# Optimization experiments

Hardware: AMD Instinct MI355X
Metric: run time of the kernel (lower is better)

Reference implementation:

```python
import jax, jax.numpy as jnp
import numpy as np

HEADS = 12
HEAD_SIZE = 64
NEG_BIG = 1e12


def _rope_sin_cos(seq_len, head_size, dtype):
    # embeddings[n, 2i] = sin(n * 10000^(-2i/d)), [n, 2i+1] = cos(...)
    pos = jnp.arange(seq_len, dtype=dtype)                      # [s]
    idx = jnp.arange(head_size // 2, dtype=dtype)               # [d/2]
    inv_freq = jnp.power(jnp.asarray(10000.0, dtype), -2.0 * idx / head_size)
    ang = jnp.einsum('n,d->nd', pos, inv_freq)                  # [s, d/2]
    # cos_pos / sin_pos: repeat_interleave each frequency twice -> [1, s, 1, d]
    cos = jnp.repeat(jnp.cos(ang), 2, axis=-1)[None, :, None, :]
    sin = jnp.repeat(jnp.sin(ang), 2, axis=-1)[None, :, None, :]
    return sin, cos


def _rotate_half_interleaved(x):
    # stack([-x[..., 1::2], x[..., ::2]], -1).reshape_as(x)
    x2 = jnp.stack([-x[..., 1::2], x[..., ::2]], axis=-1)
    return x2.reshape(x.shape)


def setup_inputs() -> dict:
    key = jax.random.key(0)
    k1, k2 = jax.random.split(key)
    bs, s, h = 16, 512, 768
    hidden = jax.random.normal(k1, (bs, s, h), dtype=jnp.float32)
    attention_mask = jnp.ones((bs, s), dtype=jnp.int32)
    W = jax.random.normal(k2, (h, HEADS * 2 * HEAD_SIZE), dtype=jnp.float32) * (h ** -0.5)
    b = jnp.zeros((HEADS * 2 * HEAD_SIZE,), dtype=jnp.float32)
    return {"hidden": hidden, "attention_mask": attention_mask, "W": W, "b": b}


def reference(hidden, attention_mask, W, b):
    bs, s, _ = hidden.shape
    x = hidden @ W + b                                           # [b, s, heads*2*hd]
    x = x.reshape(bs, s, HEADS, 2, HEAD_SIZE)
    qw, kw = x[..., 0, :], x[..., 1, :]                          # [b, s, h, d]

    sin, cos = _rope_sin_cos(s, HEAD_SIZE, hidden.dtype)
    qw = qw * cos + _rotate_half_interleaved(qw) * sin
    kw = kw * cos + _rotate_half_interleaved(kw) * sin

    logits = jnp.einsum('bmhd,bnhd->bhmn', qw, kw)               # [b, h, s, s]

    am = attention_mask.astype(logits.dtype)
    pad_mask = 1.0 - am[:, None, None, :] * am[:, None, :, None]
    logits = logits - pad_mask * NEG_BIG

    tril = jnp.tril(jnp.ones((s, s), dtype=logits.dtype), k=-1)  # strictly lower
    logits = logits - tril[None, None, :, :] * NEG_BIG

    return logits / (HEAD_SIZE ** 0.5)
```

## Files before the change

kernel.cpp:

```cpp
#include <hip/hip_runtime.h>
#include <math.h>

#define HEADS 12
#define HSZ   64
#define SEQ   512
#define HID   768
#define NOUT  1536
#define NEGQ  1.25e11f

typedef _Float16 f16x8 __attribute__((ext_vector_type(8)));
typedef _Float16 f16x4 __attribute__((ext_vector_type(4)));
typedef float    f32x4 __attribute__((ext_vector_type(4)));
typedef int      i32x4 __attribute__((ext_vector_type(4)));
typedef int      i32x8 __attribute__((ext_vector_type(8)));

__device__ __forceinline__ void async_ld16(const void* g, void* l) {
  __builtin_amdgcn_global_load_lds(
      (__attribute__((address_space(1))) void*)g,
      (__attribute__((address_space(3))) void*)l, 16, 0, 0);
}

__global__ __launch_bounds__(256) void prep_k(
    const float* __restrict__ hidden, const float* __restrict__ W,
    unsigned char* __restrict__ Xb8, unsigned char* __restrict__ Wt8,
    float2* __restrict__ tab)
{
  __shared__ float t_lds[32][33];
  const int b = blockIdx.x;
  const int t = threadIdx.x;
  if (b < 1152) {
    const int tk = b % 24, tn = b / 24;
    const int k0 = tk * 32, n0 = tn * 32;
    const int tx = t & 31, ty = t >> 5;
#pragma unroll
    for (int r = 0; r < 4; ++r)
      t_lds[ty + r * 8][tx] = W[(size_t)(k0 + ty + r * 8) * NOUT + n0 + tx];
    __syncthreads();
    const int nl = t >> 3, kg = t & 7;
    int w = __builtin_amdgcn_cvt_pk_fp8_f32(t_lds[kg * 4 + 0][nl],
                                            t_lds[kg * 4 + 1][nl], 0, false);
    w = __builtin_amdgcn_cvt_pk_fp8_f32(t_lds[kg * 4 + 2][nl],
                                        t_lds[kg * 4 + 3][nl], w, true);
    *(int*)&Wt8[(size_t)(n0 + nl) * HID + k0 + kg * 4] = w;
  } else if (b < 1152 + 1536) {
    const int idx = (b - 1152) * 256 + t;
    const float4* src = (const float4*)hidden + (size_t)idx * 4;
    float4 v0 = src[0], v1 = src[1], v2 = src[2], v3 = src[3];
    int4 o;
    o.x = __builtin_amdgcn_cvt_pk_fp8_f32(v0.x, v0.y, 0, false);
    o.x = __builtin_amdgcn_cvt_pk_fp8_f32(v0.z, v0.w, o.x, true);
    o.y = __builtin_amdgcn_cvt_pk_fp8_f32(v1.x, v1.y, 0, false);
    o.y = __builtin_amdgcn_cvt_pk_fp8_f32(v1.z, v1.w, o.y, true);
    o.z = __builtin_amdgcn_cvt_pk_fp8_f32(v2.x, v2.y, 0, false);
    o.z = __builtin_amdgcn_cvt_pk_fp8_f32(v2.z, v2.w, o.z, true);
    o.w = __builtin_amdgcn_cvt_pk_fp8_f32(v3.x, v3.y, 0, false);
    o.w = __builtin_amdgcn_cvt_pk_fp8_f32(v3.z, v3.w, o.w, true);
    ((int4*)Xb8)[idx] = o;
  } else {
    const int e = (b - 2688) * 256 + t;
    const int si = e >> 5, fi = e & 31;
    float inv = powf(10000.f, -(float)fi / 32.f);
    float ang = (float)si * inv;
    float sv, cv;
    sincosf(ang, &sv, &cv);
    tab[e] = make_float2(cv, sv);
  }
}

__global__ __launch_bounds__(256) void gemm1_k(
    const unsigned char* __restrict__ Xb8, const unsigned char* __restrict__ Wt8,
    const float* __restrict__ bias, const float2* __restrict__ tab,
    _Float16* __restrict__ qb, _Float16* __restrict__ kb)
{
  __shared__ __align__(16) int As4[4096];
  __shared__ __align__(16) int Bs4[4096];
  const int tid = threadIdx.x;
  const int lane = tid & 63;
  const int m0 = blockIdx.x * 128;
  const int n0 = blockIdx.y * 128;
  const int wm = ((tid >> 6) & 1) * 64;
  const int wn = (tid >> 7) * 64;
  const int lrow = lane & 15;
  const int q = lane >> 4;

  f32x4 acc[4][4] = {};

  for (int kt = 0; kt < 6; ++kt) {
    const int kbase = kt * 128;
#pragma unroll
    for (int c = 0; c < 4; ++c) {
      const int s = tid + c * 256;
      const int row = s >> 3, cc = s & 7;
      const int so = (((cc >> 1) ^ (row & 3)) << 5) + ((cc & 1) << 4);
      async_ld16(Xb8 + (size_t)(m0 + row) * HID + kbase + so, (char*)As4 + s * 16);
      async_ld16(Wt8 + (size_t)(n0 + row) * HID + kbase + so, (char*)Bs4 + s * 16);
    }
    __syncthreads();
    i32x8 af[4], bf[4];
#pragma unroll
    for (int i = 0; i < 4; ++i) {
      const int ra = wm + i * 16 + lrow;
      const int oa = ra * 32 + ((q ^ (ra & 3)) << 3);
      i32x4 lo = *(const i32x4*)&As4[oa];
      i32x4 hi = *(const i32x4*)&As4[oa + 4];
      af[i] = (i32x8){lo.x, lo.y, lo.z, lo.w, hi.x, hi.y, hi.z, hi.w};
      const int rb = wn + i * 16 + lrow;
      const int ob = rb * 32 + ((q ^ (rb & 3)) << 3);
      lo = *(const i32x4*)&Bs4[ob];
      hi = *(const i32x4*)&Bs4[ob + 4];
      bf[i] = (i32x8){lo.x, lo.y, lo.z, lo.w, hi.x, hi.y, hi.z, hi.w};
    }
#pragma unroll
    for (int i = 0; i < 4; ++i)
#pragma unroll
      for (int j = 0; j < 4; ++j)
        acc[i][j] = __builtin_amdgcn_mfma_scale_f32_16x16x128_f8f6f4(
            bf[j], af[i], acc[i][j], 0, 0,
            0, 0x7F7F7F7F, 0, 0x7F7F7F7F);
    __syncthreads();
  }

  const int qlane = lane >> 4;
  const int mlane = m0 + wm + (lane & 15);
#pragma unroll
  for (int j = 0; j < 4; ++j) {
    const int nb = n0 + wn + j * 16 + qlane * 4;
    const float4 b4 = *(const float4*)&bias[nb];
    const int d0 = nb & 63;
    const int h = nb >> 7;
    _Float16* dst = ((nb >> 6) & 1) ? kb : qb;
    const int fi0 = d0 >> 1;
#pragma unroll
    for (int i = 0; i < 4; ++i) {
      const int m = mlane + i * 16;
      const int si = m & (SEQ - 1);
      const int bb = m >> 9;
      const float4 cs = *(const float4*)&tab[si * 32 + fi0];
      const float v0 = acc[i][j][0] + b4.x;
      const float v1 = acc[i][j][1] + b4.y;
      const float v2 = acc[i][j][2] + b4.z;
      const float v3 = acc[i][j][3] + b4.w;
      f16x4 o;
      o.x = (_Float16)fmaf(v0, cs.x, -v1 * cs.y);
      o.y = (_Float16)fmaf(v1, cs.x, v0 * cs.y);
      o.z = (_Float16)fmaf(v2, cs.z, -v3 * cs.w);
      o.w = (_Float16)fmaf(v3, cs.z, v2 * cs.w);
      *(f16x4*)&dst[((size_t)(bb * HEADS + h) * SEQ + si) * HSZ + d0] = o;
    }
  }
}

__global__ __launch_bounds__(256) void gemm2_k(
    const _Float16* __restrict__ qb, const _Float16* __restrict__ kb,
    const int* __restrict__ am, float* __restrict__ out)
{
  const int tid = threadIdx.x;
  const int bh = blockIdx.y;
  const int bb = bh / HEADS;
  const int mt = blockIdx.x >> 2, nt = blockIdx.x & 3;
  const int m0 = mt * 128, n0 = nt * 128;
  const int* amb = am + bb * SEQ;
  float* obase = out + (size_t)bh * SEQ * SEQ;

  if (nt < mt) {
#pragma unroll
    for (int p = 0; p < 16; ++p) {
      const int f = p * 256 + tid;
      const int row = f >> 5, c4 = (f & 31) * 4;
      const int m = m0 + row;
      const float amm = (float)amb[m];
      const int nb = n0 + c4;
      const int4 a4 = *(const int4*)&amb[nb];
      f32x4 v;
      v[0] = -(2.f - amm * (float)a4.x) * NEGQ;
      v[1] = -(2.f - amm * (float)a4.y) * NEGQ;
      v[2] = -(2.f - amm * (float)a4.z) * NEGQ;
      v[3] = -(2.f - amm * (float)a4.w) * NEGQ;
      __builtin_nontemporal_store(v, (f32x4*)&obase[(size_t)m * SEQ + nb]);
    }
    return;
  }

  const _Float16* qg = qb + (size_t)bh * SEQ * HSZ;
  const _Float16* kg = kb + (size_t)bh * SEQ * HSZ;
  const int lane = tid & 63;
  const int wm = ((tid >> 6) & 1) * 64;
  const int wn = (tid >> 7) * 64;
  const int lrow = lane & 15;
  const int lk = (lane >> 4) * 8;

  f16x8 af[4][2], bf[4][2];
#pragma unroll
  for (int i = 0; i < 4; ++i)
#pragma unroll
    for (int h = 0; h < 2; ++h) {
      af[i][h] = *(const f16x8*)(qg + (size_t)(m0 + wm + i * 16 + lrow) * HSZ + h * 32 + lk);
      bf[i][h] = *(const f16x8*)(kg + (size_t)(n0 + wn + i * 16 + lrow) * HSZ + h * 32 + lk);
    }

  f32x4 acc[4][4] = {};
#pragma unroll
  for (int h = 0; h < 2; ++h)
#pragma unroll
    for (int i = 0; i < 4; ++i)
#pragma unroll
      for (int j = 0; j < 4; ++j)
        acc[i][j] = __builtin_amdgcn_mfma_f32_16x16x32_f16(bf[j][h], af[i][h], acc[i][j], 0, 0, 0);

  const int qlane = lane >> 4;
  const int mlane = m0 + wm + (lane & 15);
#pragma unroll
  for (int i = 0; i < 4; ++i) {
    const int m = mlane + i * 16;
    const float amm = (float)amb[m];
    float* orow = obase + (size_t)m * SEQ;
#pragma unroll
    for (int j = 0; j < 4; ++j) {
      const int nb = n0 + wn + j * 16 + qlane * 4;
      const int4 a4 = *(const int4*)&amb[nb];
      f32x4 v;
      v[0] = fmaf(acc[i][j][0], 0.125f,
                  -((float)(nb + 0 < m) + (1.f - amm * (float)a4.x)) * NEGQ);
      v[1] = fmaf(acc[i][j][1], 0.125f,
                  -((float)(nb + 1 < m) + (1.f - amm * (float)a4.y)) * NEGQ);
      v[2] = fmaf(acc[i][j][2], 0.125f,
                  -((float)(nb + 2 < m) + (1.f - amm * (float)a4.z)) * NEGQ);
      v[3] = fmaf(acc[i][j][3], 0.125f,
                  -((float)(nb + 3 < m) + (1.f - amm * (float)a4.w)) * NEGQ);
      __builtin_nontemporal_store(v, (f32x4*)&orow[nb]);
    }
  }
}

extern "C" void kernel_launch(void* const* d_in, const int* in_sizes, int n_in,
                              void* d_out, int out_size, void* d_ws, size_t ws_size,
                              hipStream_t stream) {
  const float* hidden = (const float*)d_in[0];
  const int*   am     = (const int*)d_in[1];
  const float* W      = (const float*)d_in[2];
  const float* bias   = (const float*)d_in[3];
  float* out = (float*)d_out;
  char* ws = (char*)d_ws;
  unsigned char* Xb8 = (unsigned char*)(ws);
  unsigned char* Wt8 = (unsigned char*)(ws + 6291456);
  _Float16* qb = (_Float16*)(ws + 7471104);
  _Float16* kb = (_Float16*)(ws + 20054016);
  float2*   tab = (float2*)(ws + 32636928);

  prep_k<<<dim3(2752), dim3(256), 0, stream>>>(hidden, W, Xb8, Wt8, tab);
  gemm1_k<<<dim3(64, 12), dim3(256), 0, stream>>>(Xb8, Wt8, bias, tab, qb, kb);
  gemm2_k<<<dim3(16, 192), dim3(256), 0, stream>>>(qb, kb, am, out);
}
```

Measured before the change: 273.3 us.

## Stage GEMM epilogues through LDS for coalesced row-contiguous global stores

Both GEMM epilogues now write their results into XOR-swizzled shared memory first, then copy whole contiguous rows out to global memory. Before, each lane stored scattered 8- or 16-byte fragments. In gemm2 the 128x128 fp32 output tile goes out in two 64-row phases through a 32 KB buffer, which adds barriers and LDS traffic. The prep kernel's hidden-to-fp8 conversion is also reshaped so each thread handles four strided float4 loads instead of four adjacent ones, to improve load coalescing.

```diff
diff --git a/kernel.cpp b/kernel.cpp
--- a/kernel.cpp
+++ b/kernel.cpp
@@ -43,19 +43,17 @@
                                         t_lds[kg * 4 + 3][nl], w, true);
     *(int*)&Wt8[(size_t)(n0 + nl) * HID + k0 + kg * 4] = w;
   } else if (b < 1152 + 1536) {
-    const int idx = (b - 1152) * 256 + t;
-    const float4* src = (const float4*)hidden + (size_t)idx * 4;
-    float4 v0 = src[0], v1 = src[1], v2 = src[2], v3 = src[3];
-    int4 o;
-    o.x = __builtin_amdgcn_cvt_pk_fp8_f32(v0.x, v0.y, 0, false);
-    o.x = __builtin_amdgcn_cvt_pk_fp8_f32(v0.z, v0.w, o.x, true);
-    o.y = __builtin_amdgcn_cvt_pk_fp8_f32(v1.x, v1.y, 0, false);
-    o.y = __builtin_amdgcn_cvt_pk_fp8_f32(v1.z, v1.w, o.y, true);
-    o.z = __builtin_amdgcn_cvt_pk_fp8_f32(v2.x, v2.y, 0, false);
-    o.z = __builtin_amdgcn_cvt_pk_fp8_f32(v2.z, v2.w, o.z, true);
-    o.w = __builtin_amdgcn_cvt_pk_fp8_f32(v3.x, v3.y, 0, false);
-    o.w = __builtin_amdgcn_cvt_pk_fp8_f32(v3.z, v3.w, o.w, true);
-    ((int4*)Xb8)[idx] = o;
+    const int base = (b - 1152) * 1024;
+    const float4* src4 = (const float4*)hidden;
+    int* dst = (int*)Xb8;
+#pragma unroll
+    for (int p = 0; p < 4; ++p) {
+      const int i = base + p * 256 + t;
+      const float4 v = src4[i];
+      int o = __builtin_amdgcn_cvt_pk_fp8_f32(v.x, v.y, 0, false);
+      o = __builtin_amdgcn_cvt_pk_fp8_f32(v.z, v.w, o, true);
+      dst[i] = o;
+    }
   } else {
     const int e = (b - 2688) * 256 + t;
     const int si = e >> 5, fi = e & 31;
@@ -120,32 +118,52 @@
     __syncthreads();
   }
 
-  const int qlane = lane >> 4;
-  const int mlane = m0 + wm + (lane & 15);
-#pragma unroll
-  for (int j = 0; j < 4; ++j) {
-    const int nb = n0 + wn + j * 16 + qlane * 4;
-    const float4 b4 = *(const float4*)&bias[nb];
-    const int d0 = nb & 63;
-    const int h = nb >> 7;
-    _Float16* dst = ((nb >> 6) & 1) ? kb : qb;
-    const int fi0 = d0 >> 1;
-#pragma unroll
-    for (int i = 0; i < 4; ++i) {
-      const int m = mlane + i * 16;
-      const int si = m & (SEQ - 1);
-      const int bb = m >> 9;
-      const float4 cs = *(const float4*)&tab[si * 32 + fi0];
-      const float v0 = acc[i][j][0] + b4.x;
-      const float v1 = acc[i][j][1] + b4.y;
-      const float v2 = acc[i][j][2] + b4.z;
-      const float v3 = acc[i][j][3] + b4.w;
-      f16x4 o;
-      o.x = (_Float16)fmaf(v0, cs.x, -v1 * cs.y);
-      o.y = (_Float16)fmaf(v1, cs.x, v0 * cs.y);
-      o.z = (_Float16)fmaf(v2, cs.z, -v3 * cs.w);
-      o.w = (_Float16)fmaf(v3, cs.z, v2 * cs.w);
-      *(f16x4*)&dst[((size_t)(bb * HEADS + h) * SEQ + si) * HSZ + d0] = o;
+  {
+    const int qlane = lane >> 4;
+    const int rbase = wm + (lane & 15);
+    f16x4* sdst = wn ? (f16x4*)Bs4 : (f16x4*)As4;
+#pragma unroll
+    for (int j = 0; j < 4; ++j) {
+      const int d0 = j * 16 + qlane * 4;
+      const int nb = n0 + wn + d0;
+      const float4 b4 = *(const float4*)&bias[nb];
+      const int fi0 = d0 >> 1;
+#pragma unroll
+      for (int i = 0; i < 4; ++i) {
+        const int r = rbase + i * 16;
+        const int m = m0 + r;
+        const int si = m & (SEQ - 1);
+        const float4 cs = *(const float4*)&tab[si * 32 + fi0];
+        const float v0 = acc[i][j][0] + b4.x;
+        const float v1 = acc[i][j][1] + b4.y;
+        const float v2 = acc[i][j][2] + b4.z;
+        const float v3 = acc[i][j][3] + b4.w;
+        f16x4 o;
+        o.x = (_Float16)fmaf(v0, cs.x, -v1 * cs.y);
+        o.y = (_Float16)fmaf(v1, cs.x, v0 * cs.y);
+        o.z = (_Float16)fmaf(v2, cs.z, -v3 * cs.w);
+        o.w = (_Float16)fmaf(v3, cs.z, v2 * cs.w);
+        sdst[r * 16 + ((d0 >> 2) ^ ((r & 7) << 1))] = o;
+      }
+    }
+  }
+  __syncthreads();
+
+  {
+    const int bb = m0 >> 9;
+    const int si0 = m0 & (SEQ - 1);
+    const int h = blockIdx.y;
+    _Float16* qdst = qb + ((size_t)(bb * HEADS + h) * SEQ + si0) * HSZ;
+    _Float16* kdst = kb + ((size_t)(bb * HEADS + h) * SEQ + si0) * HSZ;
+#pragma unroll
+    for (int p = 0; p < 4; ++p) {
+      const int idx = p * 256 + tid;
+      const int row = idx >> 3, v = idx & 7;
+      const int sv = v ^ (row & 7);
+      f16x8 qv = ((const f16x8*)As4)[row * 8 + sv];
+      f16x8 kv = ((const f16x8*)Bs4)[row * 8 + sv];
+      *(f16x8*)(qdst + row * HSZ + v * 8) = qv;
+      *(f16x8*)(kdst + row * HSZ + v * 8) = kv;
     }
   }
 }
@@ -154,6 +172,7 @@
     const _Float16* __restrict__ qb, const _Float16* __restrict__ kb,
     const int* __restrict__ am, float* __restrict__ out)
 {
+  __shared__ __align__(16) float sbuf[64 * 128];
   const int tid = threadIdx.x;
   const int bh = blockIdx.y;
   const int bb = bh / HEADS;
@@ -208,27 +227,44 @@
         acc[i][j] = __builtin_amdgcn_mfma_f32_16x16x32_f16(bf[j][h], af[i][h], acc[i][j], 0, 0, 0);
 
   const int qlane = lane >> 4;
-  const int mlane = m0 + wm + (lane & 15);
-#pragma unroll
-  for (int i = 0; i < 4; ++i) {
-    const int m = mlane + i * 16;
-    const float amm = (float)amb[m];
-    float* orow = obase + (size_t)m * SEQ;
-#pragma unroll
-    for (int j = 0; j < 4; ++j) {
-      const int nb = n0 + wn + j * 16 + qlane * 4;
-      const int4 a4 = *(const int4*)&amb[nb];
-      f32x4 v;
-      v[0] = fmaf(acc[i][j][0], 0.125f,
-                  -((float)(nb + 0 < m) + (1.f - amm * (float)a4.x)) * NEGQ);
-      v[1] = fmaf(acc[i][j][1], 0.125f,
-                  -((float)(nb + 1 < m) + (1.f - amm * (float)a4.y)) * NEGQ);
-      v[2] = fmaf(acc[i][j][2], 0.125f,
-                  -((float)(nb + 2 < m) + (1.f - amm * (float)a4.z)) * NEGQ);
-      v[3] = fmaf(acc[i][j][3], 0.125f,
-                  -((float)(nb + 3 < m) + (1.f - amm * (float)a4.w)) * NEGQ);
-      __builtin_nontemporal_store(v, (f32x4*)&orow[nb]);
-    }
+  const int rloc = lane & 15;
+  const int wmp = wm >> 6;
+  for (int ph = 0; ph < 2; ++ph) {
+    if (wmp == ph) {
+#pragma unroll
+      for (int i = 0; i < 4; ++i) {
+        const int r = i * 16 + rloc;
+        const int m = m0 + wm + r;
+        const float amm = (float)amb[m];
+#pragma unroll
+        for (int j = 0; j < 4; ++j) {
+          const int nb = n0 + wn + j * 16 + qlane * 4;
+          const int4 a4 = *(const int4*)&amb[nb];
+          f32x4 v;
+          v[0] = fmaf(acc[i][j][0], 0.125f,
+                      -((float)(nb + 0 < m) + (1.f - amm * (float)a4.x)) * NEGQ);
+          v[1] = fmaf(acc[i][j][1], 0.125f,
+                      -((float)(nb + 1 < m) + (1.f - amm * (float)a4.y)) * NEGQ);
+          v[2] = fmaf(acc[i][j][2], 0.125f,
+                      -((float)(nb + 2 < m) + (1.f - amm * (float)a4.z)) * NEGQ);
+          v[3] = fmaf(acc[i][j][3], 0.125f,
+                      -((float)(nb + 3 < m) + (1.f - amm * (float)a4.w)) * NEGQ);
+          const int t = ((wn >> 2) + j * 4 + qlane) ^ (r & 7);
+          *(f32x4*)&sbuf[r * 128 + t * 4] = v;
+        }
+      }
+    }
+    __syncthreads();
+    const int rowbase = m0 + ph * 64;
+#pragma unroll
+    for (int p = 0; p < 8; ++p) {
+      const int idx = p * 256 + tid;
+      const int row = idx >> 5, t = idx & 31;
+      f32x4 v = *(const f32x4*)&sbuf[row * 128 + ((t ^ (row & 7)) * 4)];
+      __builtin_nontemporal_store(
+          v, (f32x4*)&obase[(size_t)(rowbase + row) * SEQ + n0 + t * 4]);
+    }
+    __syncthreads();
   }
 }
 
```

Measured after the change: 266.3 us. 2.6% less time.

## Fuse projection GEMM and QK^T logits into one per-head kernel

Applied to the files above, without the earlier changes.

The projection GEMM (with bias and RoPE) and the QK^T logits kernel are merged into one kernel with one 512-thread block per (batch, head). Each block computes the full 512x128 Q/K slice, keeps the rotated fp16 Q and K in swizzled LDS, then walks the 16 output tiles with a fixed per-wave-group schedule to write logits and mask tiles. This removes the qb/kb round trip through global memory and one launch. The cost is that only 192 blocks run, each with a large LDS footprint, so occupancy and parallelism drop sharply, and every block reloads the hidden rows for its batch. The hidden-to-fp8 conversion loop is also restructured to use coalesced float4 strides.

```diff
diff --git a/kernel.cpp b/kernel.cpp
--- a/kernel.cpp
+++ b/kernel.cpp
@@ -43,19 +43,17 @@
                                         t_lds[kg * 4 + 3][nl], w, true);
     *(int*)&Wt8[(size_t)(n0 + nl) * HID + k0 + kg * 4] = w;
   } else if (b < 1152 + 1536) {
-    const int idx = (b - 1152) * 256 + t;
-    const float4* src = (const float4*)hidden + (size_t)idx * 4;
-    float4 v0 = src[0], v1 = src[1], v2 = src[2], v3 = src[3];
-    int4 o;
-    o.x = __builtin_amdgcn_cvt_pk_fp8_f32(v0.x, v0.y, 0, false);
-    o.x = __builtin_amdgcn_cvt_pk_fp8_f32(v0.z, v0.w, o.x, true);
-    o.y = __builtin_amdgcn_cvt_pk_fp8_f32(v1.x, v1.y, 0, false);
-    o.y = __builtin_amdgcn_cvt_pk_fp8_f32(v1.z, v1.w, o.y, true);
-    o.z = __builtin_amdgcn_cvt_pk_fp8_f32(v2.x, v2.y, 0, false);
-    o.z = __builtin_amdgcn_cvt_pk_fp8_f32(v2.z, v2.w, o.z, true);
-    o.w = __builtin_amdgcn_cvt_pk_fp8_f32(v3.x, v3.y, 0, false);
-    o.w = __builtin_amdgcn_cvt_pk_fp8_f32(v3.z, v3.w, o.w, true);
-    ((int4*)Xb8)[idx] = o;
+    const int base = (b - 1152) * 1024;
+    const float4* src4 = (const float4*)hidden;
+    int* dst = (int*)Xb8;
+#pragma unroll
+    for (int p = 0; p < 4; ++p) {
+      const int i = base + p * 256 + t;
+      const float4 v = src4[i];
+      int o = __builtin_amdgcn_cvt_pk_fp8_f32(v.x, v.y, 0, false);
+      o = __builtin_amdgcn_cvt_pk_fp8_f32(v.z, v.w, o, true);
+      dst[i] = o;
+    }
   } else {
     const int e = (b - 2688) * 256 + t;
     const int si = e >> 5, fi = e & 31;
@@ -67,167 +65,173 @@
   }
 }
 
-__global__ __launch_bounds__(256) void gemm1_k(
+__global__ __launch_bounds__(512) void mega_k(
     const unsigned char* __restrict__ Xb8, const unsigned char* __restrict__ Wt8,
     const float* __restrict__ bias, const float2* __restrict__ tab,
-    _Float16* __restrict__ qb, _Float16* __restrict__ kb)
+    const int* __restrict__ am, float* __restrict__ out)
 {
-  __shared__ __align__(16) int As4[4096];
-  __shared__ __align__(16) int Bs4[4096];
+  __shared__ __align__(16) int As8[16384];
+  __shared__ __align__(16) int Bs8[4096];
+  __shared__ __align__(16) int Ks[16384];
+
   const int tid = threadIdx.x;
   const int lane = tid & 63;
-  const int m0 = blockIdx.x * 128;
-  const int n0 = blockIdx.y * 128;
-  const int wm = ((tid >> 6) & 1) * 64;
-  const int wn = (tid >> 7) * 64;
+  const int w = tid >> 6;
+  const int bh = (blockIdx.x & 7) * 24 + (blockIdx.x >> 3);
+  const int bb = bh / HEADS, h = bh % HEADS;
+
   const int lrow = lane & 15;
   const int q = lane >> 4;
-
-  f32x4 acc[4][4] = {};
-
+  const int wm64 = w * 64;
+
+  f32x4 acc[4][8] = {};
   for (int kt = 0; kt < 6; ++kt) {
     const int kbase = kt * 128;
 #pragma unroll
-    for (int c = 0; c < 4; ++c) {
-      const int s = tid + c * 256;
+    for (int p = 0; p < 8; ++p) {
+      const int s = p * 512 + tid;
       const int row = s >> 3, cc = s & 7;
       const int so = (((cc >> 1) ^ (row & 3)) << 5) + ((cc & 1) << 4);
-      async_ld16(Xb8 + (size_t)(m0 + row) * HID + kbase + so, (char*)As4 + s * 16);
-      async_ld16(Wt8 + (size_t)(n0 + row) * HID + kbase + so, (char*)Bs4 + s * 16);
+      async_ld16(Xb8 + (size_t)(bb * SEQ + row) * HID + kbase + so, (char*)As8 + s * 16);
+    }
+#pragma unroll
+    for (int p = 0; p < 2; ++p) {
+      const int s = p * 512 + tid;
+      const int row = s >> 3, cc = s & 7;
+      const int so = (((cc >> 1) ^ (row & 3)) << 5) + ((cc & 1) << 4);
+      async_ld16(Wt8 + (size_t)(h * 128 + row) * HID + kbase + so, (char*)Bs8 + s * 16);
     }
     __syncthreads();
-    i32x8 af[4], bf[4];
+    i32x8 af[4];
 #pragma unroll
     for (int i = 0; i < 4; ++i) {
-      const int ra = wm + i * 16 + lrow;
+      const int ra = wm64 + i * 16 + lrow;
       const int oa = ra * 32 + ((q ^ (ra & 3)) << 3);
-      i32x4 lo = *(const i32x4*)&As4[oa];
-      i32x4 hi = *(const i32x4*)&As4[oa + 4];
+      i32x4 lo = *(const i32x4*)&As8[oa];
+      i32x4 hi = *(const i32x4*)&As8[oa + 4];
       af[i] = (i32x8){lo.x, lo.y, lo.z, lo.w, hi.x, hi.y, hi.z, hi.w};
-      const int rb = wn + i * 16 + lrow;
+    }
+#pragma unroll
+    for (int j = 0; j < 8; ++j) {
+      const int rb = j * 16 + lrow;
       const int ob = rb * 32 + ((q ^ (rb & 3)) << 3);
-      lo = *(const i32x4*)&Bs4[ob];
-      hi = *(const i32x4*)&Bs4[ob + 4];
-      bf[i] = (i32x8){lo.x, lo.y, lo.z, lo.w, hi.x, hi.y, hi.z, hi.w};
-    }
+      i32x4 lo = *(const i32x4*)&Bs8[ob];
+      i32x4 hi = *(const i32x4*)&Bs8[ob + 4];
+      i32x8 bf = (i32x8){lo.x, lo.y, lo.z, lo.w, hi.x, hi.y, hi.z, hi.w};
+#pragma unroll
+      for (int i = 0; i < 4; ++i)
+        acc[i][j] = __builtin_amdgcn_mfma_scale_f32_16x16x128_f8f6f4(
+            bf, af[i], acc[i][j], 0, 0,
+            0, 0x7F7F7F7F, 0, 0x7F7F7F7F);
+    }
+    __syncthreads();
+  }
+
+  {
+    f16x4* qdst = (f16x4*)As8;
+    f16x4* kdst = (f16x4*)Ks;
+#pragma unroll
+    for (int j = 0; j < 8; ++j) {
+      const int n = j * 16 + q * 4;
+      const int d0 = n & 63;
+      const float4 b4 = *(const float4*)&bias[h * 128 + n];
+      const int fi0 = d0 >> 1;
+      f16x4* sdst = (j >= 4) ? kdst : qdst;
+#pragma unroll
+      for (int i = 0; i < 4; ++i) {
+        const int r = wm64 + i * 16 + lrow;
+        const float4 cs = *(const float4*)&tab[r * 32 + fi0];
+        const float v0 = acc[i][j][0] + b4.x;
+        const float v1 = acc[i][j][1] + b4.y;
+        const float v2 = acc[i][j][2] + b4.z;
+        const float v3 = acc[i][j][3] + b4.w;
+        f16x4 o;
+        o.x = (_Float16)fmaf(v0, cs.x, -v1 * cs.y);
+        o.y = (_Float16)fmaf(v1, cs.x, v0 * cs.y);
+        o.z = (_Float16)fmaf(v2, cs.z, -v3 * cs.w);
+        o.w = (_Float16)fmaf(v3, cs.z, v2 * cs.w);
+        sdst[r * 16 + ((d0 >> 2) ^ ((r & 7) << 1))] = o;
+      }
+    }
+  }
+  __syncthreads();
+
+  const unsigned long long sched = (w >> 2) ? 0x0E0D0C0F0B070302ULL
+                                            : 0x0908040A06050100ULL;
+  const int t256 = tid & 255;
+  const int* amb = am + bb * SEQ;
+  float* obase = out + (size_t)bh * SEQ * SEQ;
+  const f16x8* q16 = (const f16x8*)As8;
+  const f16x8* k16 = (const f16x8*)Ks;
+  const int wm = ((t256 >> 6) & 1) * 64;
+  const int wn = (t256 >> 7) * 64;
+
+  for (int stp = 0; stp < 8; ++stp) {
+    const int te = (int)((sched >> (stp * 8)) & 15);
+    const int mt = te >> 2, nt = te & 3;
+    const int m0 = mt * 128, n0 = nt * 128;
+
+    if (nt < mt) {
+#pragma unroll
+      for (int p = 0; p < 16; ++p) {
+        const int f = p * 256 + t256;
+        const int row = f >> 5, c4 = (f & 31) * 4;
+        const int m = m0 + row;
+        const float amm = (float)amb[m];
+        const int nbf = n0 + c4;
+        const int4 a4 = *(const int4*)&amb[nbf];
+        f32x4 v;
+        v[0] = -(2.f - amm * (float)a4.x) * NEGQ;
+        v[1] = -(2.f - amm * (float)a4.y) * NEGQ;
+        v[2] = -(2.f - amm * (float)a4.z) * NEGQ;
+        v[3] = -(2.f - amm * (float)a4.w) * NEGQ;
+        __builtin_nontemporal_store(v, (f32x4*)&obase[(size_t)m * SEQ + nbf]);
+      }
+      continue;
+    }
+
+    f16x8 af2[4][2], bf2[4][2];
 #pragma unroll
     for (int i = 0; i < 4; ++i)
 #pragma unroll
-      for (int j = 0; j < 4; ++j)
-        acc[i][j] = __builtin_amdgcn_mfma_scale_f32_16x16x128_f8f6f4(
-            bf[j], af[i], acc[i][j], 0, 0,
-            0, 0x7F7F7F7F, 0, 0x7F7F7F7F);
-    __syncthreads();
-  }
-
-  const int qlane = lane >> 4;
-  const int mlane = m0 + wm + (lane & 15);
-#pragma unroll
-  for (int j = 0; j < 4; ++j) {
-    const int nb = n0 + wn + j * 16 + qlane * 4;
-    const float4 b4 = *(const float4*)&bias[nb];
-    const int d0 = nb & 63;
-    const int h = nb >> 7;
-    _Float16* dst = ((nb >> 6) & 1) ? kb : qb;
-    const int fi0 = d0 >> 1;
+      for (int hh = 0; hh < 2; ++hh) {
+        const int rA = m0 + wm + i * 16 + lrow;
+        af2[i][hh] = q16[rA * 8 + ((hh * 4 + q) ^ (rA & 7))];
+        const int rB = n0 + wn + i * 16 + lrow;
+        bf2[i][hh] = k16[rB * 8 + ((hh * 4 + q) ^ (rB & 7))];
+      }
+
+    f32x4 acc2[4][4] = {};
+#pragma unroll
+    for (int hh = 0; hh < 2; ++hh)
+#pragma unroll
+      for (int i = 0; i < 4; ++i)
+#pragma unroll
+        for (int j = 0; j < 4; ++j)
+          acc2[i][j] = __builtin_amdgcn_mfma_f32_16x16x32_f16(
+              bf2[j][hh], af2[i][hh], acc2[i][j], 0, 0, 0);
+
+    const int mlane = m0 + wm + lrow;
 #pragma unroll
     for (int i = 0; i < 4; ++i) {
       const int m = mlane + i * 16;
-      const int si = m & (SEQ - 1);
-      const int bb = m >> 9;
-      const float4 cs = *(const float4*)&tab[si * 32 + fi0];
-      const float v0 = acc[i][j][0] + b4.x;
-      const float v1 = acc[i][j][1] + b4.y;
-      const float v2 = acc[i][j][2] + b4.z;
-      const float v3 = acc[i][j][3] + b4.w;
-      f16x4 o;
-      o.x = (_Float16)fmaf(v0, cs.x, -v1 * cs.y);
-      o.y = (_Float16)fmaf(v1, cs.x, v0 * cs.y);
-      o.z = (_Float16)fmaf(v2, cs.z, -v3 * cs.w);
-      o.w = (_Float16)fmaf(v3, cs.z, v2 * cs.w);
-      *(f16x4*)&dst[((size_t)(bb * HEADS + h) * SEQ + si) * HSZ + d0] = o;
-    }
-  }
-}
-
-__global__ __launch_bounds__(256) void gemm2_k(
-    const _Float16* __restrict__ qb, const _Float16* __restrict__ kb,
-    const int* __restrict__ am, float* __restrict__ out)
-{
-  const int tid = threadIdx.x;
-  const int bh = blockIdx.y;
-  const int bb = bh / HEADS;
-  const int mt = blockIdx.x >> 2, nt = blockIdx.x & 3;
-  const int m0 = mt * 128, n0 = nt * 128;
-  const int* amb = am + bb * SEQ;
-  float* obase = out + (size_t)bh * SEQ * SEQ;
-
-  if (nt < mt) {
-#pragma unroll
-    for (int p = 0; p < 16; ++p) {
-      const int f = p * 256 + tid;
-      const int row = f >> 5, c4 = (f & 31) * 4;
-      const int m = m0 + row;
       const float amm = (float)amb[m];
-      const int nb = n0 + c4;
-      const int4 a4 = *(const int4*)&amb[nb];
-      f32x4 v;
-      v[0] = -(2.f - amm * (float)a4.x) * NEGQ;
-      v[1] = -(2.f - amm * (float)a4.y) * NEGQ;
-      v[2] = -(2.f - amm * (float)a4.z) * NEGQ;
-      v[3] = -(2.f - amm * (float)a4.w) * NEGQ;
-      __builtin_nontemporal_store(v, (f32x4*)&obase[(size_t)m * SEQ + nb]);
-    }
-    return;
-  }
-
-  const _Float16* qg = qb + (size_t)bh * SEQ * HSZ;
-  const _Float16* kg = kb + (size_t)bh * SEQ * HSZ;
-  const int lane = tid & 63;
-  const int wm = ((tid >> 6) & 1) * 64;
-  const int wn = (tid >> 7) * 64;
-  const int lrow = lane & 15;
-  const int lk = (lane >> 4) * 8;
-
-  f16x8 af[4][2], bf[4][2];
-#pragma unroll
-  for (int i = 0; i < 4; ++i)
-#pragma unroll
-    for (int h = 0; h < 2; ++h) {
-      af[i][h] = *(const f16x8*)(qg + (size_t)(m0 + wm + i * 16 + lrow) * HSZ + h * 32 + lk);
-      bf[i][h] = *(const f16x8*)(kg + (size_t)(n0 + wn + i * 16 + lrow) * HSZ + h * 32 + lk);
-    }
-
-  f32x4 acc[4][4] = {};
-#pragma unroll
-  for (int h = 0; h < 2; ++h)
-#pragma unroll
-    for (int i = 0; i < 4; ++i)
-#pragma unroll
-      for (int j = 0; j < 4; ++j)
-        acc[i][j] = __builtin_amdgcn_mfma_f32_16x16x32_f16(bf[j][h], af[i][h], acc[i][j], 0, 0, 0);
-
-  const int qlane = lane >> 4;
-  const int mlane = m0 + wm + (lane & 15);
-#pragma unroll
-  for (int i = 0; i < 4; ++i) {
-    const int m = mlane + i * 16;
-    const float amm = (float)amb[m];
-    float* orow = obase + (size_t)m * SEQ;
-#pragma unroll
-    for (int j = 0; j < 4; ++j) {
-      const int nb = n0 + wn + j * 16 + qlane * 4;
-      const int4 a4 = *(const int4*)&amb[nb];
-      f32x4 v;
-      v[0] = fmaf(acc[i][j][0], 0.125f,
-                  -((float)(nb + 0 < m) + (1.f - amm * (float)a4.x)) * NEGQ);
-      v[1] = fmaf(acc[i][j][1], 0.125f,
-                  -((float)(nb + 1 < m) + (1.f - amm * (float)a4.y)) * NEGQ);
-      v[2] = fmaf(acc[i][j][2], 0.125f,
-                  -((float)(nb + 2 < m) + (1.f - amm * (float)a4.z)) * NEGQ);
-      v[3] = fmaf(acc[i][j][3], 0.125f,
-                  -((float)(nb + 3 < m) + (1.f - amm * (float)a4.w)) * NEGQ);
-      __builtin_nontemporal_store(v, (f32x4*)&orow[nb]);
+      float* orow = obase + (size_t)m * SEQ;
+#pragma unroll
+      for (int j = 0; j < 4; ++j) {
+        const int nb = n0 + wn + j * 16 + q * 4;
+        const int4 a4 = *(const int4*)&amb[nb];
+        f32x4 v;
+        v[0] = fmaf(acc2[i][j][0], 0.125f,
+                    -((float)(nb + 0 < m) + (1.f - amm * (float)a4.x)) * NEGQ);
+        v[1] = fmaf(acc2[i][j][1], 0.125f,
+                    -((float)(nb + 1 < m) + (1.f - amm * (float)a4.y)) * NEGQ);
+        v[2] = fmaf(acc2[i][j][2], 0.125f,
+                    -((float)(nb + 2 < m) + (1.f - amm * (float)a4.z)) * NEGQ);
+        v[3] = fmaf(acc2[i][j][3], 0.125f,
+                    -((float)(nb + 3 < m) + (1.f - amm * (float)a4.w)) * NEGQ);
+        __builtin_nontemporal_store(v, (f32x4*)&orow[nb]);
+      }
     }
   }
 }
@@ -243,11 +247,8 @@
   char* ws = (char*)d_ws;
   unsigned char* Xb8 = (unsigned char*)(ws);
   unsigned char* Wt8 = (unsigned char*)(ws + 6291456);
-  _Float16* qb = (_Float16*)(ws + 7471104);
-  _Float16* kb = (_Float16*)(ws + 20054016);
-  float2*   tab = (float2*)(ws + 32636928);
+  float2*   tab = (float2*)(ws + 7471104);
 
   prep_k<<<dim3(2752), dim3(256), 0, stream>>>(hidden, W, Xb8, Wt8, tab);
-  gemm1_k<<<dim3(64, 12), dim3(256), 0, stream>>>(Xb8, Wt8, bias, tab, qb, kb);
-  gemm2_k<<<dim3(16, 192), dim3(256), 0, stream>>>(qb, kb, am, out);
-}
+  mega_k<<<dim3(192), dim3(512), 0, stream>>>(Xb8, Wt8, bias, tab, am, out);
+}
```

After: 282.7 us. +3.4%, slower.
